# Optimization experiments

Hardware: AMD Instinct MI355X
Metric: run time of the kernel (lower is better)

The kernel has to match this reference:

```python
import jax, jax.numpy as jnp
import numpy as np

VOCAB = 100000
E = 300          # embedding_size
S = 128          # seq_len
B = 8192         # batch
H1 = 2048
H2 = 2048
C = 1221         # num_classes
PAD = 1          # padding token id (sentence trimmed after last non-1 token)


def setup_inputs() -> dict:
    key = jax.random.key(0)
    ks = jax.random.split(key, 8)
    x = jax.random.randint(ks[0], (S, B), 0, VOCAB, dtype=jnp.int64 if jax.config.jax_enable_x64 else jnp.int32)
    emb = jax.random.normal(ks[1], (VOCAB, E), dtype=jnp.float32) * 0.1
    W1 = jax.random.normal(ks[2], (H1, 2 * E), dtype=jnp.float32) * (1.0 / np.sqrt(2 * E))
    b1 = jnp.zeros((H1,), dtype=jnp.float32)
    W2 = jax.random.normal(ks[3], (H2, H1), dtype=jnp.float32) * (1.0 / np.sqrt(H1))
    b2 = jnp.zeros((H2,), dtype=jnp.float32)
    W_out = jax.random.normal(ks[4], (C, H2), dtype=jnp.float32) * (1.0 / np.sqrt(H2))
    b_out = jnp.zeros((C,), dtype=jnp.float32)
    return {"x": x, "emb": emb, "W1": W1, "b1": b1, "W2": W2, "b2": b2,
            "W_out": W_out, "b_out": b_out}


def reference(x, emb, W1, b1, W2, b2, W_out, b_out):
    # x: [S, B] token ids -> transpose to [B, S] as in torch forward
    xb = x.T                                   # [B, S]
    nonpad = xb != PAD                         # [B, S]
    # index of LAST non-padding token per sentence (torch: (sent != 1).nonzero()[-1])
    last = (S - 1) - jnp.argmax(nonpad[:, ::-1], axis=1)      # [B]
    pos = jnp.arange(S)
    # sentence[:last+1] keeps everything up to and including `last`,
    # including any PAD tokens inside that prefix (faithful to the slice).
    mask = (pos[None, :] <= last[:, None]).astype(emb.dtype)  # [B, S]

    ex = emb[xb]                               # [B, S, E] embedding lookup
    mean = jnp.einsum('bse,bs->be', ex, mask) / jnp.sum(mask, axis=1, keepdims=True)
    feat = jnp.concatenate([ex[:, 0, :], mean], axis=1)       # [B, 2E] (FEE + avg)

    h = jax.nn.relu(feat @ W1.T + b1)          # [B, H1]
    h = jax.nn.relu(h @ W2.T + b2)             # [B, H2]
    out = h @ W_out.T + b_out                  # [B, C]
    return out
```

## Files before the change

kernel.cpp:

```cpp
#include <hip/hip_runtime.h>
#include <hip/hip_bf16.h>

#define S 128
#define BATCH 8192
#define E 300
#define KPAD 640
#define H1 2048
#define H2 2048
#define CLS 1221
#define CPAD 1280
#define PADTOK 1
#define VOCAB 100000

typedef __bf16 bf16x8 __attribute__((ext_vector_type(8)));
typedef float f32x4 __attribute__((ext_vector_type(4)));

__device__ __forceinline__ float b2f(ushort u) {
  union { unsigned int i; float f; } v; v.i = ((unsigned int)u) << 16; return v.f;
}
__device__ __forceinline__ ushort f2b(float f) {
  unsigned int i = __float_as_uint(f);
  unsigned int r = (i + 0x7FFFu + ((i >> 16) & 1u)) >> 16;
  return (ushort)r;
}
__device__ __forceinline__ void async16(const void* g, void* l) {
  __builtin_amdgcn_global_load_lds(
      (__attribute__((address_space(1))) void*)(void*)(const_cast<void*>(g)),
      (__attribute__((address_space(3))) void*)l, 16, 0, 0);
}

#define NQ_EMB (VOCAB * E / 4)
#define NQ_W1  (H1 * KPAD / 4)
#define NQ_W2  (H1 * H2 / 4)
#define NQ_WO  (CPAD * H2 / 4)
#define NQ_XT  (S * BATCH / 4)
#define NQ_TOT (NQ_EMB + NQ_W1 + NQ_W2 + NQ_WO + NQ_XT)

__global__ __launch_bounds__(256) void cvt_all(const float* __restrict__ Ein,
                                               ushort* __restrict__ Eb,
                                               const float* __restrict__ W1,
                                               ushort* __restrict__ W1p,
                                               const float* __restrict__ W2,
                                               ushort* __restrict__ W2b,
                                               const float* __restrict__ Wout,
                                               ushort* __restrict__ Woutp,
                                               const int* __restrict__ x,
                                               int* __restrict__ xT) {
  int q = blockIdx.x * 256 + threadIdx.x;
  if (q < NQ_EMB) {
    float4 v = ((const float4*)Ein)[q];
    ushort4 o;
    o.x = f2b(v.x); o.y = f2b(v.y); o.z = f2b(v.z); o.w = f2b(v.w);
    ((ushort4*)Eb)[q] = o;
    return;
  }
  q -= NQ_EMB;
  if (q < NQ_W1) {
    int row = q / 160;
    int k0 = (q - row * 160) * 4;
    ushort4 o; o.x = 0; o.y = 0; o.z = 0; o.w = 0;
    if (k0 < 2 * E) {
      float4 v = *(const float4*)(W1 + (size_t)row * (2 * E) + k0);
      o.x = f2b(v.x); o.y = f2b(v.y); o.z = f2b(v.z); o.w = f2b(v.w);
    }
    ((ushort4*)W1p)[q] = o;
    return;
  }
  q -= NQ_W1;
  if (q < NQ_W2) {
    float4 v = ((const float4*)W2)[q];
    ushort4 o;
    o.x = f2b(v.x); o.y = f2b(v.y); o.z = f2b(v.z); o.w = f2b(v.w);
    ((ushort4*)W2b)[q] = o;
    return;
  }
  q -= NQ_W2;
  if (q < NQ_WO) {
    int n = (q * 4) >> 11;
    ushort4 o; o.x = 0; o.y = 0; o.z = 0; o.w = 0;
    if (n < CLS) {
      float4 v = ((const float4*)Wout)[q];
      o.x = f2b(v.x); o.y = f2b(v.y); o.z = f2b(v.z); o.w = f2b(v.w);
    }
    ((ushort4*)Woutp)[q] = o;
    return;
  }
  q -= NQ_WO;
  if (q < NQ_XT) {
    int b = q >> 5;
    int t4 = (q & 31) * 4;
    int4 o;
    o.x = x[(size_t)(t4 + 0) * BATCH + b];
    o.y = x[(size_t)(t4 + 1) * BATCH + b];
    o.z = x[(size_t)(t4 + 2) * BATCH + b];
    o.w = x[(size_t)(t4 + 3) * BATCH + b];
    ((int4*)xT)[q] = o;
  }
}

__global__ __launch_bounds__(128) void embed_kernel(const int* __restrict__ xT,
                                                    const ushort* __restrict__ emb,
                                                    ushort* __restrict__ feat) {
  __shared__ uint offs[S];
  __shared__ unsigned long long masks[2];
  __shared__ __align__(16) float part[76 * 4];
  const int b = blockIdx.x;
  const int t = threadIdx.x;

  int tok = xT[b * S + t];
  offs[t] = (uint)tok * 600u;
  unsigned long long m = __ballot(tok != PADTOK);
  if ((t & 63) == 0) masks[t >> 6] = m;
  __syncthreads();

  unsigned long long m0 = masks[0], m1 = masks[1];
  int last;
  if (m1)      last = 127 - __clzll(m1);
  else if (m0) last = 63 - __clzll(m0);
  else         last = S - 1;
  const int n = last + 1;
  const float inv = 1.0f / (float)n;

  const int w = t >> 6;
  const int lane = t & 63;
  const char* base = (const char*)emb;
  const uint off0 = (uint)lane * 8u;
  const bool tail = (lane < 11);
  const uint off1 = 512u + (uint)lane * 8u;

  float a0 = 0.f, a1 = 0.f, a2 = 0.f, a3 = 0.f;
  float c0 = 0.f, c1 = 0.f, c2 = 0.f, c3 = 0.f;

  int s = w;
  for (; s + 14 < n; s += 16) {
    uint o[8];
#pragma unroll
    for (int j = 0; j < 8; j++) o[j] = offs[s + 2 * j];
    ushort4 u[8];
#pragma unroll
    for (int j = 0; j < 8; j++) u[j] = *(const ushort4*)(base + (o[j] + off0));
    ushort4 v[8];
    if (tail) {
#pragma unroll
      for (int j = 0; j < 8; j++) v[j] = *(const ushort4*)(base + (o[j] + off1));
    }
#pragma unroll
    for (int j = 0; j < 8; j++) {
      a0 += b2f(u[j].x); a1 += b2f(u[j].y);
      a2 += b2f(u[j].z); a3 += b2f(u[j].w);
    }
    if (tail) {
#pragma unroll
      for (int j = 0; j < 8; j++) {
        c0 += b2f(v[j].x); c1 += b2f(v[j].y);
        c2 += b2f(v[j].z); c3 += b2f(v[j].w);
      }
    }
  }
  for (; s < n; s += 2) {
    uint o = offs[s];
    ushort4 u = *(const ushort4*)(base + (o + off0));
    a0 += b2f(u.x); a1 += b2f(u.y); a2 += b2f(u.z); a3 += b2f(u.w);
    if (tail) {
      ushort4 v = *(const ushort4*)(base + (o + off1));
      c0 += b2f(v.x); c1 += b2f(v.y); c2 += b2f(v.z); c3 += b2f(v.w);
    }
  }

  if (w == 1) {
    float4 av; av.x = a0; av.y = a1; av.z = a2; av.w = a3;
    *(float4*)&part[lane * 4] = av;
    if (tail) {
      float4 cv; cv.x = c0; cv.y = c1; cv.z = c2; cv.w = c3;
      *(float4*)&part[(64 + lane) * 4] = cv;
    }
  }
  __syncthreads();

  ushort* fr = feat + (size_t)b * KPAD;
  if (w == 0) {
    float4 pv = *(const float4*)&part[lane * 4];
    ushort4 mo;
    mo.x = f2b((a0 + pv.x) * inv); mo.y = f2b((a1 + pv.y) * inv);
    mo.z = f2b((a2 + pv.z) * inv); mo.w = f2b((a3 + pv.w) * inv);
    *(ushort4*)(fr + E + lane * 4) = mo;
    if (tail) {
      float4 qv = *(const float4*)&part[(64 + lane) * 4];
      ushort4 mo2;
      mo2.x = f2b((c0 + qv.x) * inv); mo2.y = f2b((c1 + qv.y) * inv);
      mo2.z = f2b((c2 + qv.z) * inv); mo2.w = f2b((c3 + qv.w) * inv);
      *(ushort4*)(fr + E + (64 + lane) * 4) = mo2;
    }
  }

  const uint o0 = offs[0];
  if (t < 75) {
    *(ushort4*)(fr + 4 * t) = *(const ushort4*)(base + (o0 + 8u * (uint)t));
  } else if (t < 85) {
    ushort4 z; z.x = 0; z.y = 0; z.z = 0; z.w = 0;
    *(ushort4*)(fr + 2 * E + 4 * (t - 75)) = z;
  }
}

#define BM2 256
#define BN2 256
#define BK2 64

__device__ __forceinline__ void stage_half(const ushort* __restrict__ P,
                                           int ld, int org, ushort* dst,
                                           int kg, int tid, int wave) {
  const int sc = tid & 3;
  const int r0 = tid >> 2;
#pragma unroll
  for (int j = 0; j < 2; ++j) {
    const int row = j * 128 + r0;
    const int c2 = sc ^ ((row >> 1) & 3);
    async16(P + (size_t)(org + row) * ld + kg + c2 * 8,
            (void*)(dst + j * 4096 + wave * 512));
  }
}

#define PH_READ_B(KH)                                                        \
  _Pragma("unroll") for (int nf = 0; nf < 4; ++nf) {                         \
    const int row = wc * 64 + nf * 16 + fr;                                  \
    bfrag[nf] = *(const bf16x8*)&sB[(KH) * 8192 + row * 32 +                 \
                                    ((fq ^ ((row >> 1) & 3)) * 8)];          \
  }
#define PH_READ_A(MH, KH)                                                    \
  _Pragma("unroll") for (int f = 0; f < 4; ++f) {                            \
    const int row = wr * 128 + (MH) * 64 + f * 16 + fr;                      \
    afrag[f] = *(const bf16x8*)&sA[(KH) * 8192 + row * 32 +                  \
                                   ((fq ^ ((row >> 1) & 3)) * 8)];           \
  }
#define PH_MFMA(MH)                                                          \
  __builtin_amdgcn_s_setprio(1);                                             \
  _Pragma("unroll") for (int f = 0; f < 4; ++f)                              \
    _Pragma("unroll") for (int nf = 0; nf < 4; ++nf)                         \
      acc[(MH) * 4 + f][nf] = __builtin_amdgcn_mfma_f32_16x16x32_bf16(       \
          afrag[f], bfrag[nf], acc[(MH) * 4 + f][nf], 0, 0, 0);              \
  __builtin_amdgcn_s_setprio(0);
#define BAR_SCHED()                                                          \
  __builtin_amdgcn_s_barrier();                                              \
  __builtin_amdgcn_sched_barrier(0);

template <bool RELU, bool NGUARD, bool FP32OUT>
__global__ __launch_bounds__(512, 2) void gemm_bt(const ushort* __restrict__ A,
                                                  const ushort* __restrict__ B,
                                                  const float* __restrict__ bias,
                                                  void* __restrict__ Cv,
                                                  int K, int lda, int ldb,
                                                  int ldc, int Nreal) {
  __shared__ __align__(16) ushort sm[65536];

  const int tid = threadIdx.x;
  const int wave = tid >> 6;
  const int lane = tid & 63;

  const int gx = gridDim.x;
  const int nwg = gx * gridDim.y;
  const int lin = blockIdx.y * gx + blockIdx.x;
  const int wsw = (lin & 7) * (nwg >> 3) + (lin >> 3);
  const int m0 = (wsw / gx) * BM2;
  const int n0 = (wsw % gx) * BN2;

  const int wr = wave >> 2;
  const int wc = wave & 3;
  const int fr = lane & 15;
  const int fq = lane >> 4;

  f32x4 acc[8][4];
#pragma unroll
  for (int i = 0; i < 8; ++i)
#pragma unroll
    for (int j = 0; j < 4; ++j)
#pragma unroll
      for (int r = 0; r < 4; ++r) acc[i][j][r] = 0.f;

  bf16x8 afrag[4], bfrag[4];
  const int NT = K / BK2;

  {
    ushort* sA0 = sm;
    ushort* sB0 = sm + 16384;
    stage_half(A, lda, m0, sA0, 0, tid, wave);
    stage_half(B, ldb, n0, sB0, 0, tid, wave);
    stage_half(A, lda, m0, sA0 + 8192, 32, tid, wave);
    stage_half(B, ldb, n0, sB0 + 8192, 32, tid, wave);
    asm volatile("s_waitcnt vmcnt(4)" ::: "memory");
    BAR_SCHED();
  }

  for (int t = 0; t < NT - 1; ++t) {
    const int s = t & 1;
    ushort* sA = sm + s * 32768;
    ushort* sB = sA + 16384;
    ushort* dA = sm + (s ^ 1) * 32768;
    ushort* dB = dA + 16384;
    const int kn = (t + 1) * BK2;

    PH_READ_B(0);
    PH_READ_A(0, 0);
    stage_half(A, lda, m0, dA, kn, tid, wave);
    BAR_SCHED();
    PH_MFMA(0);
    BAR_SCHED();

    PH_READ_A(1, 0);
    stage_half(B, ldb, n0, dB, kn, tid, wave);
    asm volatile("s_waitcnt vmcnt(4)" ::: "memory");
    BAR_SCHED();
    PH_MFMA(1);
    BAR_SCHED();

    PH_READ_B(1);
    PH_READ_A(0, 1);
    stage_half(A, lda, m0, dA + 8192, kn + 32, tid, wave);
    BAR_SCHED();
    PH_MFMA(0);
    BAR_SCHED();

    PH_READ_A(1, 1);
    stage_half(B, ldb, n0, dB + 8192, kn + 32, tid, wave);
    asm volatile("s_waitcnt vmcnt(4)" ::: "memory");
    BAR_SCHED();
    PH_MFMA(1);
    BAR_SCHED();
  }

  {
    const int s = (NT - 1) & 1;
    ushort* sA = sm + s * 32768;
    ushort* sB = sA + 16384;

    PH_READ_B(0);
    PH_READ_A(0, 0);
    BAR_SCHED();
    PH_MFMA(0);
    BAR_SCHED();

    PH_READ_A(1, 0);
    asm volatile("s_waitcnt vmcnt(0)" ::: "memory");
    BAR_SCHED();
    PH_MFMA(1);
    BAR_SCHED();

    PH_READ_B(1);
    PH_READ_A(0, 1);
    BAR_SCHED();
    PH_MFMA(0);
    BAR_SCHED();

    PH_READ_A(1, 1);
    PH_MFMA(1);
  }

#pragma unroll
  for (int nf = 0; nf < 4; ++nf) {
    const int col = n0 + wc * 64 + nf * 16 + fr;
    const bool ok = (!NGUARD) || (col < Nreal);
    const float bv = ok ? bias[col] : 0.f;
#pragma unroll
    for (int g = 0; g < 8; ++g) {
      const int rbase = m0 + wr * 128 + (g >> 2) * 64 + (g & 3) * 16 + fq * 4;
#pragma unroll
      for (int rr = 0; rr < 4; ++rr) {
        const int row = rbase + rr;
        float v = acc[g][nf][rr] + bv;
        if (RELU) v = fmaxf(v, 0.f);
        if (ok) {
          if (FP32OUT) ((float*)Cv)[(size_t)row * ldc + col] = v;
          else         ((ushort*)Cv)[(size_t)row * ldc + col] = f2b(v);
        }
      }
    }
  }
}

extern "C" void kernel_launch(void* const* d_in, const int* in_sizes, int n_in,
                              void* d_out, int out_size, void* d_ws, size_t ws_size,
                              hipStream_t stream) {
  const int* x = (const int*)d_in[0];
  const float* emb = (const float*)d_in[1];
  const float* W1 = (const float*)d_in[2];
  const float* b1 = (const float*)d_in[3];
  const float* W2 = (const float*)d_in[4];
  const float* b2 = (const float*)d_in[5];
  const float* Wout = (const float*)d_in[6];
  const float* bout = (const float*)d_in[7];
  float* out = (float*)d_out;

  char* ws = (char*)d_ws;
  ushort* feat = (ushort*)ws;  ws += (size_t)BATCH * KPAD * 2;
  ushort* h1 = (ushort*)ws;    ws += (size_t)BATCH * H1 * 2;
  ushort* h2 = (ushort*)ws;    ws += (size_t)BATCH * H2 * 2;
  ushort* W1p = (ushort*)ws;   ws += (size_t)H1 * KPAD * 2;
  ushort* W2b = (ushort*)ws;   ws += (size_t)H2 * H1 * 2;
  ushort* Woutp = (ushort*)ws; ws += (size_t)CPAD * H2 * 2;
  ushort* Eb = (ushort*)ws;    ws += (size_t)VOCAB * E * 2;
  int* xT = (int*)ws;          ws += (size_t)S * BATCH * 4;

  cvt_all<<<(NQ_TOT + 255) / 256, 256, 0, stream>>>(emb, Eb, W1, W1p, W2, W2b,
                                                    Wout, Woutp, x, xT);
  embed_kernel<<<BATCH, S, 0, stream>>>(xT, Eb, feat);

  gemm_bt<true, false, false><<<dim3(H1 / BN2, BATCH / BM2), 512, 0, stream>>>(
      feat, W1p, b1, (void*)h1, KPAD, KPAD, KPAD, H1, H1);
  gemm_bt<true, false, false><<<dim3(H2 / BN2, BATCH / BM2), 512, 0, stream>>>(
      h1, W2b, b2, (void*)h2, H1, H1, H1, H2, H2);
  gemm_bt<false, true, true><<<dim3(CPAD / BN2, BATCH / BM2), 512, 0, stream>>>(
      h2, Woutp, bout, (void*)out, H2, H2, H2, CLS, CLS);
}
```

Before: 492.5 us.

## Restructure GEMM mainloop into 4-stage BK=32 ring-buffer pipeline

```diff
diff --git a/kernel.cpp b/kernel.cpp
--- a/kernel.cpp
+++ b/kernel.cpp
@@ -204,11 +204,11 @@
 
 #define BM2 256
 #define BN2 256
-#define BK2 64
-
-__device__ __forceinline__ void stage_half(const ushort* __restrict__ P,
-                                           int ld, int org, ushort* dst,
-                                           int kg, int tid, int wave) {
+#define BK2 32
+
+__device__ __forceinline__ void stage32(const ushort* __restrict__ P,
+                                        int ld, int org, ushort* dst,
+                                        int kg, int tid, int wave) {
   const int sc = tid & 3;
   const int r0 = tid >> 2;
 #pragma unroll
@@ -220,16 +220,16 @@
   }
 }
 
-#define PH_READ_B(KH)                                                        \
+#define PH_READ_B()                                                          \
   _Pragma("unroll") for (int nf = 0; nf < 4; ++nf) {                         \
     const int row = wc * 64 + nf * 16 + fr;                                  \
-    bfrag[nf] = *(const bf16x8*)&sB[(KH) * 8192 + row * 32 +                 \
+    bfrag[nf] = *(const bf16x8*)&sB[row * 32 +                               \
                                     ((fq ^ ((row >> 1) & 3)) * 8)];          \
   }
-#define PH_READ_A(MH, KH)                                                    \
+#define PH_READ_A(MH)                                                        \
   _Pragma("unroll") for (int f = 0; f < 4; ++f) {                            \
     const int row = wr * 128 + (MH) * 64 + f * 16 + fr;                      \
-    afrag[f] = *(const bf16x8*)&sA[(KH) * 8192 + row * 32 +                  \
+    afrag[f] = *(const bf16x8*)&sA[row * 32 +                                \
                                    ((fq ^ ((row >> 1) & 3)) * 8)];           \
   }
 #define PH_MFMA(MH)                                                          \
@@ -280,77 +280,74 @@
   const int NT = K / BK2;
 
   {
-    ushort* sA0 = sm;
-    ushort* sB0 = sm + 16384;
-    stage_half(A, lda, m0, sA0, 0, tid, wave);
-    stage_half(B, ldb, n0, sB0, 0, tid, wave);
-    stage_half(A, lda, m0, sA0 + 8192, 32, tid, wave);
-    stage_half(B, ldb, n0, sB0 + 8192, 32, tid, wave);
+    stage32(A, lda, m0, sm,                 0, tid, wave);
+    stage32(B, ldb, n0, sm + 8192,          0, tid, wave);
+    stage32(A, lda, m0, sm + 16384,        32, tid, wave);
+    stage32(B, ldb, n0, sm + 16384 + 8192, 32, tid, wave);
+    stage32(A, lda, m0, sm + 32768,        64, tid, wave);
+    stage32(B, ldb, n0, sm + 32768 + 8192, 64, tid, wave);
+    asm volatile("s_waitcnt vmcnt(8)" ::: "memory");
+    BAR_SCHED();
+  }
+
+  for (int t = 0; t <= NT - 4; ++t) {
+    const ushort* sA = sm + (t & 3) * 16384;
+    const ushort* sB = sA + 8192;
+    ushort* dst = sm + ((t + 3) & 3) * 16384;
+    const int kn = (t + 3) * BK2;
+
+    PH_READ_B();
+    PH_READ_A(0);
+    stage32(A, lda, m0, dst, kn, tid, wave);
+    BAR_SCHED();
+    PH_MFMA(0);
+    BAR_SCHED();
+
+    PH_READ_A(1);
+    stage32(B, ldb, n0, dst + 8192, kn, tid, wave);
+    asm volatile("s_waitcnt vmcnt(8)" ::: "memory");
+    BAR_SCHED();
+    PH_MFMA(1);
+    BAR_SCHED();
+  }
+
+  {
+    const ushort* sA = sm + ((NT - 3) & 3) * 16384;
+    const ushort* sB = sA + 8192;
+    PH_READ_B();
+    PH_READ_A(0);
+    BAR_SCHED();
+    PH_MFMA(0);
+    BAR_SCHED();
+    PH_READ_A(1);
     asm volatile("s_waitcnt vmcnt(4)" ::: "memory");
     BAR_SCHED();
-  }
-
-  for (int t = 0; t < NT - 1; ++t) {
-    const int s = t & 1;
-    ushort* sA = sm + s * 32768;
-    ushort* sB = sA + 16384;
-    ushort* dA = sm + (s ^ 1) * 32768;
-    ushort* dB = dA + 16384;
-    const int kn = (t + 1) * BK2;
-
-    PH_READ_B(0);
-    PH_READ_A(0, 0);
-    stage_half(A, lda, m0, dA, kn, tid, wave);
+    PH_MFMA(1);
+    BAR_SCHED();
+  }
+  {
+    const ushort* sA = sm + ((NT - 2) & 3) * 16384;
+    const ushort* sB = sA + 8192;
+    PH_READ_B();
+    PH_READ_A(0);
     BAR_SCHED();
     PH_MFMA(0);
     BAR_SCHED();
-
-    PH_READ_A(1, 0);
-    stage_half(B, ldb, n0, dB, kn, tid, wave);
-    asm volatile("s_waitcnt vmcnt(4)" ::: "memory");
+    PH_READ_A(1);
+    asm volatile("s_waitcnt vmcnt(0)" ::: "memory");
     BAR_SCHED();
     PH_MFMA(1);
     BAR_SCHED();
-
-    PH_READ_B(1);
-    PH_READ_A(0, 1);
-    stage_half(A, lda, m0, dA + 8192, kn + 32, tid, wave);
+  }
+  {
+    const ushort* sA = sm + ((NT - 1) & 3) * 16384;
+    const ushort* sB = sA + 8192;
+    PH_READ_B();
+    PH_READ_A(0);
     BAR_SCHED();
     PH_MFMA(0);
     BAR_SCHED();
-
-    PH_READ_A(1, 1);
-    stage_half(B, ldb, n0, dB + 8192, kn + 32, tid, wave);
-    asm volatile("s_waitcnt vmcnt(4)" ::: "memory");
-    BAR_SCHED();
-    PH_MFMA(1);
-    BAR_SCHED();
-  }
-
-  {
-    const int s = (NT - 1) & 1;
-    ushort* sA = sm + s * 32768;
-    ushort* sB = sA + 16384;
-
-    PH_READ_B(0);
-    PH_READ_A(0, 0);
-    BAR_SCHED();
-    PH_MFMA(0);
-    BAR_SCHED();
-
-    PH_READ_A(1, 0);
-    asm volatile("s_waitcnt vmcnt(0)" ::: "memory");
-    BAR_SCHED();
-    PH_MFMA(1);
-    BAR_SCHED();
-
-    PH_READ_B(1);
-    PH_READ_A(0, 1);
-    BAR_SCHED();
-    PH_MFMA(0);
-    BAR_SCHED();
-
-    PH_READ_A(1, 1);
+    PH_READ_A(1);
     PH_MFMA(1);
   }
 
```

New measurement: 490.9 us. Within noise of the previous version (-0.3%).
